# Kernel tuning notes

Hardware: AMD Instinct MI355X
Metric: run time of the kernel (lower is better)

The kernel has to match this reference:

```python
import jax, jax.numpy as jnp
import numpy as np

F = 16      # frames
NV = 4096   # visual points per frame
NT = 512    # tactile points per frame
M = 4096    # model points
SCALE = 0.1


def setup_inputs() -> dict:
    key = jax.random.key(0)
    ks = jax.random.split(key, 6)
    return {
        "state": jax.random.normal(ks[0], (6,), dtype=jnp.float32) * 0.1,
        "model_points": jax.random.normal(ks[1], (M, 3), dtype=jnp.float32),
        "visual_points": jax.random.normal(ks[2], (F, NV, 3), dtype=jnp.float32),
        "tactile_points": jax.random.normal(ks[3], (F, NT, 3), dtype=jnp.float32),
        "physics_pred_states": jax.random.normal(ks[4], (F, 12), dtype=jnp.float32) * 0.1,
        "delta_time": jax.random.uniform(ks[5], (F,), dtype=jnp.float32, minval=0.01, maxval=0.05),
    }


def _skew(a):
    z = jnp.zeros((), a.dtype)
    return jnp.array([[z, -a[2], a[1]],
                      [a[2], z, -a[0]],
                      [-a[1], a[0], z]])


def _rot_from_omega(omega, dt):
    # Rodrigues: R = I + sin(theta*dt) S + (1 - cos(theta*dt)) S@S, S = skew(omega/|omega|)
    theta = jnp.linalg.norm(omega)
    ax = omega / jnp.clip(theta, 1e-8)
    S = _skew(ax)
    return jnp.eye(3, dtype=omega.dtype) + jnp.sin(theta * dt) * S + (1.0 - jnp.cos(theta * dt)) * (S @ S)


def _chamfer(pred, gt):
    # rows: pred [N,3], cols: gt [M,3]; row-min of squared distances, then mean
    d = (jnp.sum(pred * pred, axis=1)[:, None]
         + jnp.sum(gt * gt, axis=1)[None, :]
         - 2.0 * pred @ gt.T)
    return jnp.mean(jnp.min(d, axis=1))


def reference(state, model_points, visual_points, tactile_points, physics_pred_states, delta_time):
    t0 = state[:3]
    r0 = _rot_from_omega(state[3:], jnp.float32(1.0))  # Euler2Mat modeled as axis-angle

    def pose_step(carry, x):
        t, r = carry
        v, omega, dt = x
        t = t + v * dt
        r = _rot_from_omega(omega, dt) @ r
        return (t, r), (t, r)

    _, (ts, rs) = jax.lax.scan(
        pose_step, (t0, r0),
        (physics_pred_states[1:, 6:9], physics_pred_states[1:, 9:12], delta_time[1:]))
    ts = jnp.concatenate([t0[None], ts], axis=0)  # [F,3]
    rs = jnp.concatenate([r0[None], rs], axis=0)  # [F,3,3]

    def frame_loss(acc, x):
        t, r, vp, tp = x
        vc = ((vp - t) @ r) / SCALE
        tc = ((tp - t) @ r) / SCALE
        acc = acc + _chamfer(vc, model_points) + 0.1 * _chamfer(tc, model_points)
        return acc, None

    E_cd, _ = jax.lax.scan(frame_loss, jnp.zeros((), jnp.float32),
                           (ts, rs, visual_points, tactile_points))
    return E_cd
```

## Files before the change

### kernel.cpp

```cpp
#include <hip/hip_runtime.h>
#include <math.h>

#define F_    16
#define NV_   4096
#define NT_   512
#define M_    4096
#define PPF_  (NV_ + NT_)
#define NPTS_ (F_ * PPF_)
#define SCALE_INV 10.0f

#define TPB     256
#define PTSB    64
#define NBLK    (NPTS_ / PTSB)
#define CHUNK   128
#define NCHUNK  (M_ / CHUNK)
#define NSPLIT  32
#define MPS     (CHUNK / NSPLIT)
#define PPT     8

__device__ inline void rot_from_omega(float ox, float oy, float oz, float dt,
                                      float* R) {
    float theta = sqrtf(ox * ox + oy * oy + oz * oz);
    float inv = 1.0f / fmaxf(theta, 1e-8f);
    float ax = ox * inv, ay = oy * inv, az = oz * inv;
    float s = sinf(theta * dt);
    float c = 1.0f - cosf(theta * dt);
    R[0] = 1.0f - c * (ay * ay + az * az);
    R[1] = -s * az + c * ax * ay;
    R[2] =  s * ay + c * ax * az;
    R[3] =  s * az + c * ax * ay;
    R[4] = 1.0f - c * (ax * ax + az * az);
    R[5] = -s * ax + c * ay * az;
    R[6] = -s * ay + c * ax * az;
    R[7] =  s * ax + c * ay * az;
    R[8] = 1.0f - c * (ax * ax + ay * ay);
}

__device__ inline void compute_pose_serial(int f, const float* state,
                                           const float* phys, const float* dts,
                                           float* t, float* R) {
    t[0] = state[0]; t[1] = state[1]; t[2] = state[2];
    rot_from_omega(state[3], state[4], state[5], 1.0f, R);
    for (int i = 1; i <= f; ++i) {
        float dt = dts[i];
        t[0] += phys[i * 12 + 6] * dt;
        t[1] += phys[i * 12 + 7] * dt;
        t[2] += phys[i * 12 + 8] * dt;
        float Rs[9];
        rot_from_omega(phys[i * 12 + 9], phys[i * 12 + 10], phys[i * 12 + 11], dt, Rs);
        float Rn[9];
        for (int r = 0; r < 3; ++r)
            for (int c2 = 0; c2 < 3; ++c2)
                Rn[r * 3 + c2] = Rs[r * 3 + 0] * R[0 + c2] +
                                 Rs[r * 3 + 1] * R[3 + c2] +
                                 Rs[r * 3 + 2] * R[6 + c2];
        for (int j = 0; j < 9; ++j) R[j] = Rn[j];
    }
}

__global__ __launch_bounds__(TPB) void chamfer_one(
    const float* __restrict__ state, const float* __restrict__ model,
    const float* __restrict__ vis, const float* __restrict__ tac,
    const float* __restrict__ phys, const float* __restrict__ dts,
    float* __restrict__ out) {
    __shared__ float4 featD[2][TPB];
    __shared__ float  sposes[F_ * 12];
    __shared__ float  sdm[PTSB][NSPLIT + 1];

    const int t = threadIdx.x;

    if (t < F_) {
        float tr[3], R[9];
        compute_pose_serial(t, state, phys, dts, tr, R);
        float* o = sposes + t * 12;
        o[0] = tr[0]; o[1] = tr[1]; o[2] = tr[2];
        for (int j = 0; j < 9; ++j) o[3 + j] = R[j] * SCALE_INV;
    }

    {
        const int mi = (t >> 3) * MPS + (t & 3);
        float gx = model[mi * 3 + 0], gy = model[mi * 3 + 1], gz = model[mi * 3 + 2];
        featD[0][t] = make_float4(-2.0f * gx, -2.0f * gy, -2.0f * gz,
                                  gx * gx + gy * gy + gz * gz);
    }
    __syncthreads();

    const int pg  = t & 7;
    const int sp  = t >> 3;
    const int rot = t & 3;
    const int f   = (blockIdx.x * PTSB) / PPF_;
    const int lbase = blockIdx.x * PTSB - f * PPF_;

    float c0[PPT], c1[PPT], c2[PPT], cn[PPT], dm[PPT];
#pragma unroll
    for (int k = 0; k < PPT; ++k) {
        int loc = lbase + pg * PPT + k;
        const float* p = (loc < NV_) ? (vis + ((size_t)f * NV_ + loc) * 3)
                                     : (tac + ((size_t)f * NT_ + (loc - NV_)) * 3);
        float px = p[0], py = p[1], pz = p[2];
        const float* ps = sposes + f * 12;
        float d0 = px - ps[0], d1 = py - ps[1], d2 = pz - ps[2];
        const float* R = ps + 3;
        float x = d0 * R[0] + d1 * R[3] + d2 * R[6];
        float y = d0 * R[1] + d1 * R[4] + d2 * R[7];
        float z = d0 * R[2] + d1 * R[5] + d2 * R[8];
        c0[k] = x; c1[k] = y; c2[k] = z;
        cn[k] = x * x + y * y + z * z;
        dm[k] = 3.4e38f;
    }

    for (int c = 0; c < NCHUNK; ++c) {
        const int cur = c & 1;
        if (c + 1 < NCHUNK) {
            const int mi = (c + 1) * CHUNK + sp * MPS + (t & 3);
            float gx = model[mi * 3 + 0], gy = model[mi * 3 + 1], gz = model[mi * 3 + 2];
            featD[cur ^ 1][t] = make_float4(-2.0f * gx, -2.0f * gy, -2.0f * gz,
                                            gx * gx + gy * gy + gz * gz);
        }
        const float4* fb = &featD[cur][sp * 8];
#pragma unroll
        for (int m = 0; m < MPS; m += 2) {
            float4 ga = fb[rot + m];
            float4 gb = fb[rot + m + 1];
#pragma unroll
            for (int k = 0; k < PPT; ++k) {
                float da = fmaf(ga.x, c0[k], fmaf(ga.y, c1[k], fmaf(ga.z, c2[k], ga.w)));
                float db = fmaf(gb.x, c0[k], fmaf(gb.y, c1[k], fmaf(gb.z, c2[k], gb.w)));
                dm[k] = fminf(dm[k], fminf(da, db));
            }
        }
        __syncthreads();
    }

#pragma unroll
    for (int k = 0; k < PPT; ++k) sdm[pg * PPT + k][sp] = dm[k] + cn[k];
    __syncthreads();

    if (t < PTSB) {
        float mn = sdm[t][0];
#pragma unroll
        for (int i = 1; i < NSPLIT; ++i) mn = fminf(mn, sdm[t][i]);
        const int loc = lbase + t;
        const float w = (loc < NV_) ? (1.0f / NV_) : (0.1f / NT_);
        float v = mn * w;
#pragma unroll
        for (int off = 32; off > 0; off >>= 1) v += __shfl_down(v, off);
        if (t == 0) atomicAdd(out, v);
    }
}

extern "C" void kernel_launch(void* const* d_in, const int* in_sizes, int n_in,
                              void* d_out, int out_size, void* d_ws, size_t ws_size,
                              hipStream_t stream) {
    const float* state = (const float*)d_in[0];
    const float* model = (const float*)d_in[1];
    const float* vis   = (const float*)d_in[2];
    const float* tac   = (const float*)d_in[3];
    const float* phys  = (const float*)d_in[4];
    const float* dts   = (const float*)d_in[5];
    float* out = (float*)d_out;
    (void)d_ws; (void)ws_size;

    hipMemsetAsync(out, 0, sizeof(float), stream);
    chamfer_one<<<NBLK, TPB, 0, stream>>>(state, model, vis, tac, phys, dts, out);
}
```

Before: 113.0 us.

## Repartition chamfer work into 8 model groups with 3 points per lane

Each block now handles 96 points instead of 64. The model set is split into 8 groups of 512 points, one per 32-lane slice, and each lane keeps 3 points in registers, so every lane in a slice reads the same broadcast shared-memory feature. Staging chunks drop from 32 to 8 per block, which cuts barriers, and the grid becomes 768 blocks, which may balance better across CUs. Per-frame rotations are now built in parallel and only the 3x3 products are chained serially in one thread. In exchange, each loaded model feature is reused across fewer points per thread, raising shared-memory reads per FMA.

```diff
diff --git a/kernel.cpp b/kernel.cpp
--- a/kernel.cpp
+++ b/kernel.cpp
@@ -9,14 +9,15 @@
 #define NPTS_ (F_ * PPF_)
 #define SCALE_INV 10.0f
 
-#define TPB     256
-#define PTSB    64
-#define NBLK    (NPTS_ / PTSB)
-#define CHUNK   128
-#define NCHUNK  (M_ / CHUNK)
-#define NSPLIT  32
-#define MPS     (CHUNK / NSPLIT)
-#define PPT     8
+#define TPB   256
+#define PTSB  96
+#define NBLK  (NPTS_ / PTSB)
+#define NMG   8
+#define MPG   (M_ / NMG)
+#define CHM   64
+#define NCH   (MPG / CHM)
+#define FS    66
+#define PPL   3
 
 __device__ inline void rot_from_omega(float ox, float oy, float oz, float dt,
                                       float* R) {
@@ -36,94 +37,116 @@
     R[8] = 1.0f - c * (ax * ax + ay * ay);
 }
 
-__device__ inline void compute_pose_serial(int f, const float* state,
-                                           const float* phys, const float* dts,
-                                           float* t, float* R) {
-    t[0] = state[0]; t[1] = state[1]; t[2] = state[2];
-    rot_from_omega(state[3], state[4], state[5], 1.0f, R);
-    for (int i = 1; i <= f; ++i) {
-        float dt = dts[i];
-        t[0] += phys[i * 12 + 6] * dt;
-        t[1] += phys[i * 12 + 7] * dt;
-        t[2] += phys[i * 12 + 8] * dt;
-        float Rs[9];
-        rot_from_omega(phys[i * 12 + 9], phys[i * 12 + 10], phys[i * 12 + 11], dt, Rs);
-        float Rn[9];
-        for (int r = 0; r < 3; ++r)
-            for (int c2 = 0; c2 < 3; ++c2)
-                Rn[r * 3 + c2] = Rs[r * 3 + 0] * R[0 + c2] +
-                                 Rs[r * 3 + 1] * R[3 + c2] +
-                                 Rs[r * 3 + 2] * R[6 + c2];
-        for (int j = 0; j < 9; ++j) R[j] = Rn[j];
-    }
-}
-
 __global__ __launch_bounds__(TPB) void chamfer_one(
     const float* __restrict__ state, const float* __restrict__ model,
     const float* __restrict__ vis, const float* __restrict__ tac,
     const float* __restrict__ phys, const float* __restrict__ dts,
     float* __restrict__ out) {
-    __shared__ float4 featD[2][TPB];
+    __shared__ float4 featD[2][NMG * FS];
     __shared__ float  sposes[F_ * 12];
-    __shared__ float  sdm[PTSB][NSPLIT + 1];
+    __shared__ float  sRs[F_ * 9];
+    __shared__ float  sdt[F_ * 3];
+    __shared__ float  sdm[PTSB][NMG + 1];
+    __shared__ float  sw[2];
 
     const int t = threadIdx.x;
 
     if (t < F_) {
-        float tr[3], R[9];
-        compute_pose_serial(t, state, phys, dts, tr, R);
-        float* o = sposes + t * 12;
-        o[0] = tr[0]; o[1] = tr[1]; o[2] = tr[2];
-        for (int j = 0; j < 9; ++j) o[3 + j] = R[j] * SCALE_INV;
+        float ox, oy, oz, dt;
+        if (t == 0) { ox = state[3]; oy = state[4]; oz = state[5]; dt = 1.0f; }
+        else        { ox = phys[t * 12 + 9]; oy = phys[t * 12 + 10];
+                      oz = phys[t * 12 + 11]; dt = dts[t]; }
+        float Rs[9];
+        rot_from_omega(ox, oy, oz, dt, Rs);
+        for (int j = 0; j < 9; ++j) sRs[t * 9 + j] = Rs[j];
+        if (t > 0) {
+            sdt[t * 3 + 0] = phys[t * 12 + 6] * dt;
+            sdt[t * 3 + 1] = phys[t * 12 + 7] * dt;
+            sdt[t * 3 + 2] = phys[t * 12 + 8] * dt;
+        }
+    }
+    if (t == 0) {
+        float R[9];
+        for (int j = 0; j < 9; ++j) R[j] = sRs[j];
+        float tr[3] = {state[0], state[1], state[2]};
+        for (int i = 0; i < F_; ++i) {
+            if (i > 0) {
+                tr[0] += sdt[i * 3 + 0];
+                tr[1] += sdt[i * 3 + 1];
+                tr[2] += sdt[i * 3 + 2];
+                float Rn[9];
+                const float* Rsp = sRs + i * 9;
+                for (int r = 0; r < 3; ++r)
+                    for (int c2 = 0; c2 < 3; ++c2)
+                        Rn[r * 3 + c2] = Rsp[r * 3 + 0] * R[0 + c2] +
+                                         Rsp[r * 3 + 1] * R[3 + c2] +
+                                         Rsp[r * 3 + 2] * R[6 + c2];
+                for (int j = 0; j < 9; ++j) R[j] = Rn[j];
+            }
+            float* o = sposes + i * 12;
+            o[0] = tr[0]; o[1] = tr[1]; o[2] = tr[2];
+            for (int j = 0; j < 9; ++j) o[3 + j] = R[j] * SCALE_INV;
+        }
     }
 
     {
-        const int mi = (t >> 3) * MPS + (t & 3);
-        float gx = model[mi * 3 + 0], gy = model[mi * 3 + 1], gz = model[mi * 3 + 2];
-        featD[0][t] = make_float4(-2.0f * gx, -2.0f * gy, -2.0f * gz,
-                                  gx * gx + gy * gy + gz * gz);
+        const int g = t >> 5, m = t & 31;
+        int id = g * MPG + m;
+        float gx = model[id * 3 + 0], gy = model[id * 3 + 1], gz = model[id * 3 + 2];
+        featD[0][g * FS + m] = make_float4(-2.0f * gx, -2.0f * gy, -2.0f * gz,
+                                           gx * gx + gy * gy + gz * gz);
+        id += 32;
+        gx = model[id * 3 + 0]; gy = model[id * 3 + 1]; gz = model[id * 3 + 2];
+        featD[0][g * FS + m + 32] = make_float4(-2.0f * gx, -2.0f * gy, -2.0f * gz,
+                                                gx * gx + gy * gy + gz * gz);
     }
     __syncthreads();
 
-    const int pg  = t & 7;
-    const int sp  = t >> 3;
-    const int rot = t & 3;
-    const int f   = (blockIdx.x * PTSB) / PPF_;
+    const int pl = t & 31;
+    const int mg = t >> 5;
+    const int f = (blockIdx.x * PTSB) / PPF_;
     const int lbase = blockIdx.x * PTSB - f * PPF_;
 
-    float c0[PPT], c1[PPT], c2[PPT], cn[PPT], dm[PPT];
+    float c0[PPL], c1[PPL], c2[PPL], cn[PPL], dm[PPL];
+    {
+        const float* ps = sposes + f * 12;
 #pragma unroll
-    for (int k = 0; k < PPT; ++k) {
-        int loc = lbase + pg * PPT + k;
-        const float* p = (loc < NV_) ? (vis + ((size_t)f * NV_ + loc) * 3)
-                                     : (tac + ((size_t)f * NT_ + (loc - NV_)) * 3);
-        float px = p[0], py = p[1], pz = p[2];
-        const float* ps = sposes + f * 12;
-        float d0 = px - ps[0], d1 = py - ps[1], d2 = pz - ps[2];
-        const float* R = ps + 3;
-        float x = d0 * R[0] + d1 * R[3] + d2 * R[6];
-        float y = d0 * R[1] + d1 * R[4] + d2 * R[7];
-        float z = d0 * R[2] + d1 * R[5] + d2 * R[8];
-        c0[k] = x; c1[k] = y; c2[k] = z;
-        cn[k] = x * x + y * y + z * z;
-        dm[k] = 3.4e38f;
+        for (int k = 0; k < PPL; ++k) {
+            int loc = lbase + k * 32 + pl;
+            const float* p = (loc < NV_) ? (vis + ((size_t)f * NV_ + loc) * 3)
+                                         : (tac + ((size_t)f * NT_ + (loc - NV_)) * 3);
+            float px = p[0], py = p[1], pz = p[2];
+            float d0 = px - ps[0], d1 = py - ps[1], d2 = pz - ps[2];
+            const float* R = ps + 3;
+            float x = d0 * R[0] + d1 * R[3] + d2 * R[6];
+            float y = d0 * R[1] + d1 * R[4] + d2 * R[7];
+            float z = d0 * R[2] + d1 * R[5] + d2 * R[8];
+            c0[k] = x; c1[k] = y; c2[k] = z;
+            cn[k] = x * x + y * y + z * z;
+            dm[k] = 3.4e38f;
+        }
     }
 
-    for (int c = 0; c < NCHUNK; ++c) {
+    for (int c = 0; c < NCH; ++c) {
         const int cur = c & 1;
-        if (c + 1 < NCHUNK) {
-            const int mi = (c + 1) * CHUNK + sp * MPS + (t & 3);
-            float gx = model[mi * 3 + 0], gy = model[mi * 3 + 1], gz = model[mi * 3 + 2];
-            featD[cur ^ 1][t] = make_float4(-2.0f * gx, -2.0f * gy, -2.0f * gz,
-                                            gx * gx + gy * gy + gz * gz);
+        if (c + 1 < NCH) {
+            const int g = t >> 5, m = t & 31;
+            int id = g * MPG + (c + 1) * CHM + m;
+            float gx = model[id * 3 + 0], gy = model[id * 3 + 1], gz = model[id * 3 + 2];
+            featD[cur ^ 1][g * FS + m] = make_float4(-2.0f * gx, -2.0f * gy, -2.0f * gz,
+                                                     gx * gx + gy * gy + gz * gz);
+            id += 32;
+            gx = model[id * 3 + 0]; gy = model[id * 3 + 1]; gz = model[id * 3 + 2];
+            featD[cur ^ 1][g * FS + m + 32] = make_float4(-2.0f * gx, -2.0f * gy, -2.0f * gz,
+                                                          gx * gx + gy * gy + gz * gz);
         }
-        const float4* fb = &featD[cur][sp * 8];
+        const float4* fb = &featD[cur][mg * FS];
 #pragma unroll
-        for (int m = 0; m < MPS; m += 2) {
-            float4 ga = fb[rot + m];
-            float4 gb = fb[rot + m + 1];
+        for (int m = 0; m < CHM; m += 2) {
+            float4 ga = fb[m];
+            float4 gb = fb[m + 1];
 #pragma unroll
-            for (int k = 0; k < PPT; ++k) {
+            for (int k = 0; k < PPL; ++k) {
                 float da = fmaf(ga.x, c0[k], fmaf(ga.y, c1[k], fmaf(ga.z, c2[k], ga.w)));
                 float db = fmaf(gb.x, c0[k], fmaf(gb.y, c1[k], fmaf(gb.z, c2[k], gb.w)));
                 dm[k] = fminf(dm[k], fminf(da, db));
@@ -133,20 +156,25 @@
     }
 
 #pragma unroll
-    for (int k = 0; k < PPT; ++k) sdm[pg * PPT + k][sp] = dm[k] + cn[k];
+    for (int k = 0; k < PPL; ++k) sdm[k * 32 + pl][mg] = dm[k] + cn[k];
     __syncthreads();
 
+    float v = 0.0f;
     if (t < PTSB) {
         float mn = sdm[t][0];
 #pragma unroll
-        for (int i = 1; i < NSPLIT; ++i) mn = fminf(mn, sdm[t][i]);
+        for (int i = 1; i < NMG; ++i) mn = fminf(mn, sdm[t][i]);
         const int loc = lbase + t;
         const float w = (loc < NV_) ? (1.0f / NV_) : (0.1f / NT_);
-        float v = mn * w;
+        v = mn * w;
+    }
+    if (t < 128) {
 #pragma unroll
         for (int off = 32; off > 0; off >>= 1) v += __shfl_down(v, off);
-        if (t == 0) atomicAdd(out, v);
+        if ((t & 63) == 0) sw[t >> 6] = v;
     }
+    __syncthreads();
+    if (t == 0) atomicAdd(out, sw[0] + sw[1]);
 }
 
 extern "C" void kernel_launch(void* const* d_in, const int* in_sizes, int n_in,
```

Result: faster. 101.3 us (-10.4%).
